# Kernel tuning notes

Hardware: AMD Instinct MI355X
Metric: run time of the kernel (lower is better)

Reference implementation:

```python
import jax, jax.numpy as jnp
import numpy as np

B = 2048   # batch
D = 1280   # backbone feature dim (hardcoded in module)
E = 8      # num_classes == number of expert heads
ALPHA = 0.1
EPS = 1e-5


def _bn(x, g, b, m, v):
    # BatchNorm1d in eval mode: running stats
    return (x - m) * jax.lax.rsqrt(v + EPS) * g + b


def _ln(x, g, b):
    mu = jnp.mean(x, axis=-1, keepdims=True)
    var = jnp.mean((x - mu) ** 2, axis=-1, keepdims=True)
    return (x - mu) * jax.lax.rsqrt(var + EPS) * g + b


@jax.custom_vjp
def _grad_reverse(x):
    return x

def _gr_fwd(x):
    return x, None

def _gr_bwd(_, g):
    return (-ALPHA * g,)

_grad_reverse.defvjp(_gr_fwd, _gr_bwd)


def setup_inputs() -> dict:
    key = jax.random.key(0)
    ks = iter(jax.random.split(key, 80))
    def w(*s):
        return jax.random.normal(next(ks), s, dtype=jnp.float32) * 0.02
    def u(*s):
        return jax.random.uniform(next(ks), s, dtype=jnp.float32) + 0.5
    inp = {"source": jax.random.normal(next(ks), (B, D), dtype=jnp.float32)}
    # bottleneck: Linear(1280,512)+BN+ReLU, Linear(512,256)+BN+ReLU
    inp.update(bw1=w(D, 512), bb1=jnp.zeros(512), bg1=jnp.ones(512), bbe1=jnp.zeros(512), bm1=w(512), bv1=u(512))
    inp.update(bw2=w(512, 256), bb2=jnp.zeros(256), bg2=jnp.ones(256), bbe2=jnp.zeros(256), bm2=w(256), bv2=u(256))
    # source_fc: Linear(256, E) + LogSoftmax
    inp.update(cw=w(256, E), cb=jnp.zeros(E))
    # domain classifier: 1280->1024->1024->512->2 with BN
    inp.update(dw1=w(D, 1024), db1=jnp.zeros(1024), dg1=jnp.ones(1024), dbe1=jnp.zeros(1024), dm1=w(1024), dv1=u(1024))
    inp.update(dw2=w(1024, 1024), db2=jnp.zeros(1024), dg2=jnp.ones(1024), dbe2=jnp.zeros(1024), dm2=w(1024), dv2=u(1024))
    inp.update(dw3=w(1024, 512), db3=jnp.zeros(512), dg3=jnp.ones(512), dbe3=jnp.zeros(512), dm3=w(512), dv3=u(512))
    inp.update(dw4=w(512, 2), db4=jnp.zeros(2))
    # E stacked expert MLPs: 1280->1024->1024->512->2 with LayerNorm
    inp.update(ew1=w(E, D, 1024), eb1=jnp.zeros((E, 1024)), eg1=jnp.ones((E, 1024)), ebe1=jnp.zeros((E, 1024)))
    inp.update(ew2=w(E, 1024, 1024), eb2=jnp.zeros((E, 1024)), eg2=jnp.ones((E, 1024)), ebe2=jnp.zeros((E, 1024)))
    inp.update(ew3=w(E, 1024, 512), eb3=jnp.zeros((E, 512)), eg3=jnp.ones((E, 512)), ebe3=jnp.zeros((E, 512)))
    inp.update(ew4=w(E, 512, 2), eb4=jnp.zeros((E, 2)))
    return inp


def reference(source, bw1, bb1, bg1, bbe1, bm1, bv1, bw2, bb2, bg2, bbe2, bm2, bv2, cw, cb,
              dw1, db1, dg1, dbe1, dm1, dv1, dw2, db2, dg2, dbe2, dm2, dv2,
              dw3, db3, dg3, dbe3, dm3, dv3, dw4, db4,
              ew1, eb1, eg1, ebe1, ew2, eb2, eg2, ebe2, ew3, eb3, eg3, ebe3, ew4, eb4):
    share = source  # sharedNet modeled as identity on extracted features
    # bottleneck + classifier head
    h = jax.nn.relu(_bn(share @ bw1 + bb1, bg1, bbe1, bm1, bv1))
    h = jax.nn.relu(_bn(h @ bw2 + bb2, bg2, bbe2, bm2, bv2))
    src = jax.nn.log_softmax(h @ cw + cb, axis=-1)            # [B, E]
    label = jnp.argmax(src, axis=-1)                          # routing labels (detached by argmax)
    # gradient-reversed features
    rev = _grad_reverse(share)
    # global domain classifier (dropout = identity in eval)
    d = jax.nn.relu(_bn(rev @ dw1 + db1, dg1, dbe1, dm1, dv1))
    d = jax.nn.relu(_bn(d @ dw2 + db2, dg2, dbe2, dm2, dv2))
    d = jax.nn.relu(_bn(d @ dw3 + db3, dg3, dbe3, dm3, dv3))
    dclf = jax.nn.log_softmax(d @ dw4 + db4, axis=-1)         # [B, 2]
    # per-class domain experts: dense all-expert compute + per-sample gather
    x = jax.nn.relu(_ln(jnp.einsum('bd,edh->beh', rev, ew1) + eb1[None], eg1[None], ebe1[None]))
    x = jax.nn.relu(_ln(jnp.einsum('beh,ehk->bek', x, ew2) + eb2[None], eg2[None], ebe2[None]))
    x = jax.nn.relu(_ln(jnp.einsum('beh,ehk->bek', x, ew3) + eb3[None], eg3[None], ebe3[None]))
    eo = jax.nn.log_softmax(jnp.einsum('beh,ehk->bek', x, ew4) + eb4[None], axis=-1)  # [B, E, 2]
    sout = jnp.take_along_axis(eo, label[:, None, None], axis=1)[:, 0, :]             # [B, 2]
    return (src, dclf, sout, share)
```

## Files before the change

### kernel.cpp

```cpp
#include <hip/hip_runtime.h>

typedef unsigned short u16;
typedef short s8v __attribute__((ext_vector_type(8)));
typedef float f4v __attribute__((ext_vector_type(4)));

#define AS1 __attribute__((address_space(1)))
#define AS3 __attribute__((address_space(3)))

__device__ __forceinline__ float bf2f(u16 u) {
    union { unsigned int i; float f; } x; x.i = ((unsigned int)u) << 16; return x.f;
}
__device__ __forceinline__ u16 f2bf(float f) {
    union { float f; unsigned int i; } x; x.f = f;
    unsigned int r = x.i + 0x7fffu + ((x.i >> 16) & 1u);
    return (u16)(r >> 16);
}

__device__ __forceinline__ void glds16(const u16* g, u16* l) {
    __builtin_amdgcn_global_load_lds((AS1 void*)(g), (AS3 void*)(l), 16, 0, 0);
}

__device__ __forceinline__ int swz(int row, int kq) {
    return row * 64 + ((((kq >> 3) ^ row) & 7) << 3);
}

__global__ __launch_bounds__(256) void convT2_k(const float* __restrict__ Wa,
        const float* __restrict__ Wb, int zSplit,
        u16* __restrict__ WT, int N, int K)
{
    const int z = blockIdx.z;
    const float* W = (z < zSplit) ? Wa + (size_t)z * K * N
                                  : Wb + (size_t)(z - zSplit) * K * N;
    WT += (size_t)z * K * N;
    const int n0 = blockIdx.x * 64, k0 = blockIdx.y * 64;
    __shared__ float t[64][65];
    const int r = threadIdx.x >> 2;
    const int c = (threadIdx.x & 3) << 4;
    const float* wp = W + (size_t)(k0 + r) * N + n0 + c;
    #pragma unroll
    for (int q = 0; q < 16; q += 4) {
        float4 f = *(const float4*)(wp + q);
        t[c + q + 0][r] = f.x; t[c + q + 1][r] = f.y;
        t[c + q + 2][r] = f.z; t[c + q + 3][r] = f.w;
    }
    __syncthreads();
    u16* op = WT + (size_t)(n0 + r) * K + k0 + c;
    #pragma unroll
    for (int q = 0; q < 16; q += 8) {
        s8v v;
        #pragma unroll
        for (int j = 0; j < 8; ++j) v[j] = (short)f2bf(t[r][c + q + j]);
        *(s8v*)(op + q) = v;
    }
}

__global__ __launch_bounds__(256) void convsrc_k(const float* __restrict__ in,
        u16* __restrict__ outb, float* __restrict__ outf, int n8)
{
    const int i = blockIdx.x * 256 + threadIdx.x;
    if (i >= n8) return;
    const float4 f0 = ((const float4*)in)[i * 2];
    const float4 f1 = ((const float4*)in)[i * 2 + 1];
    s8v v;
    v[0]=(short)f2bf(f0.x); v[1]=(short)f2bf(f0.y);
    v[2]=(short)f2bf(f0.z); v[3]=(short)f2bf(f0.w);
    v[4]=(short)f2bf(f1.x); v[5]=(short)f2bf(f1.y);
    v[6]=(short)f2bf(f1.z); v[7]=(short)f2bf(f1.w);
    ((s8v*)outb)[i] = v;
    ((float4*)outf)[i * 2]     = f0;
    ((float4*)outf)[i * 2 + 1] = f1;
}

__device__ __forceinline__ void stage_tile(u16* AsH, u16* BsH,
        const u16* ga, const u16* gb, int kk, int ldsq, int K)
{
    #pragma unroll
    for (int q = 0; q < 4; ++q) {
        glds16(ga + kk + (size_t)q * 32 * K, AsH + q * 2048 + ldsq);
        glds16(gb + kk + (size_t)q * 32 * K, BsH + q * 2048 + ldsq);
    }
}

template<int HASDOM>
__global__ __launch_bounds__(256) void gemm_bt128_k(
    const u16* __restrict__ A0, size_t aStrideZ,
    const u16* __restrict__ WT0,
    const float* __restrict__ ebias,
    const float* __restrict__ dbias, const float* __restrict__ dgam,
    const float* __restrict__ dbet,  const float* __restrict__ dmean,
    const float* __restrict__ dvar,  int zdom,
    u16* __restrict__ out0, int M, int N, int K)
{
    const int z = blockIdx.z;
    const u16* A  = A0  + (size_t)z * aStrideZ;
    const u16* WT = WT0 + (size_t)z * N * K;
    u16* out = out0 + (size_t)z * M * N;

    const int n0 = blockIdx.x * 128, m0 = blockIdx.y * 128;
    const int t = threadIdx.x;
    const int w = t >> 6, lane = t & 63;
    const int lq = lane >> 4, lr = lane & 15;
    const int wm = (w >> 1) * 64, wn = (w & 1) * 64;

    __shared__ __align__(16) u16 As[2 * 128 * 64];
    __shared__ __align__(16) u16 Bs[2 * 128 * 64];

    f4v acc[4][4] = {};

    const int schunk = ((t & 7) ^ ((t >> 3) & 7)) << 3;
    const u16* ga = A  + (size_t)(m0 + (t >> 3)) * K + schunk;
    const u16* gb = WT + (size_t)(n0 + (t >> 3)) * K + schunk;
    const int ldsq = w * 512;

    const int NT = K >> 6;
    stage_tile(As, Bs, ga, gb, 0, ldsq, K);
    if (NT > 1) stage_tile(As + 8192, Bs + 8192, ga, gb, 64, ldsq, K);

    for (int tk = 0; tk < NT; ++tk) {
        if (tk < NT - 1) asm volatile("s_waitcnt vmcnt(8)" ::: "memory");
        else             asm volatile("s_waitcnt vmcnt(0)" ::: "memory");
        __builtin_amdgcn_s_barrier();
        __builtin_amdgcn_sched_barrier(0);

        const u16* Ah = As + (tk & 1) * 8192;
        const u16* Bh = Bs + (tk & 1) * 8192;
        __builtin_amdgcn_s_setprio(1);
        #pragma unroll
        for (int ks = 0; ks < 64; ks += 32) {
            const int kq = ks + (lq << 3);
            s8v a[4], b[4];
            #pragma unroll
            for (int i = 0; i < 4; ++i) a[i] = *(const s8v*)&Ah[swz(wm + i*16 + lr, kq)];
            #pragma unroll
            for (int j = 0; j < 4; ++j) b[j] = *(const s8v*)&Bh[swz(wn + j*16 + lr, kq)];
            #pragma unroll
            for (int i = 0; i < 4; ++i)
                #pragma unroll
                for (int j = 0; j < 4; ++j)
                    acc[i][j] = __builtin_amdgcn_mfma_f32_16x16x32_bf16(a[i], b[j], acc[i][j], 0, 0, 0);
        }
        __builtin_amdgcn_s_setprio(0);
        __builtin_amdgcn_sched_barrier(0);
        __builtin_amdgcn_s_barrier();

        if (tk + 2 < NT)
            stage_tile(As + (tk & 1) * 8192, Bs + (tk & 1) * 8192,
                       ga, gb, (tk + 2) << 6, ldsq, K);
    }

    float scale[4], shift[4];
    const bool dom = HASDOM && (z == zdom);
    #pragma unroll
    for (int j = 0; j < 4; ++j) {
        const int c = n0 + wn + j * 16 + lr;
        if (dom) {
            const float s = dgam[c] / sqrtf(dvar[c] + 1e-5f);
            scale[j] = s;
            shift[j] = (dbias[c] - dmean[c]) * s + dbet[c];
        } else {
            scale[j] = 1.f;
            shift[j] = ebias[(size_t)z * N + c];
        }
    }
    const int r0 = lq << 2;
    #pragma unroll
    for (int i = 0; i < 4; ++i) {
        #pragma unroll
        for (int r = 0; r < 4; ++r) {
            const int grow = m0 + wm + i * 16 + r0 + r;
            u16* orow = out + (size_t)grow * N + n0 + wn + lr;
            #pragma unroll
            for (int j = 0; j < 4; ++j) {
                float y = fmaf(acc[i][j][r], scale[j], shift[j]);
                if (dom) y = fmaxf(y, 0.f);
                orow[j * 16] = f2bf(y);
            }
        }
    }
}

__global__ __launch_bounds__(256) void gemm_f32sk_k(
    const float* __restrict__ A, const float* __restrict__ W,
    float* __restrict__ out, int M, int N, int K, int Ks)
{
    const int n0 = blockIdx.x * 64, m0 = blockIdx.y * 64;
    const int kb = blockIdx.z * Ks;
    out += (size_t)blockIdx.z * M * N;
    const int tid = threadIdx.x;
    const int tx = tid & 15, ty = tid >> 4;
    __shared__ float As[64][65];
    __shared__ float Bs[64][64];
    float acc[4][4] = {};
    const int sr = tid >> 2;
    const int sc = (tid & 3) << 4;
    for (int kk = kb; kk < kb + Ks; kk += 64) {
        const float* ap = A + (size_t)(m0 + sr) * K + kk + sc;
        #pragma unroll
        for (int q = 0; q < 4; ++q) {
            float4 f = *(const float4*)(ap + q * 4);
            As[sr][sc + q*4 + 0] = f.x; As[sr][sc + q*4 + 1] = f.y;
            As[sr][sc + q*4 + 2] = f.z; As[sr][sc + q*4 + 3] = f.w;
        }
        const float* wp = W + (size_t)(kk + sr) * N + n0 + sc;
        #pragma unroll
        for (int q = 0; q < 4; ++q)
            *(float4*)&Bs[sr][sc + q*4] = *(const float4*)(wp + q * 4);
        __syncthreads();
        #pragma unroll 4
        for (int kq = 0; kq < 64; ++kq) {
            float a[4], bv[4];
            #pragma unroll
            for (int i = 0; i < 4; ++i) a[i] = As[ty*4 + i][kq];
            #pragma unroll
            for (int j = 0; j < 4; ++j) bv[j] = Bs[kq][tx*4 + j];
            #pragma unroll
            for (int i = 0; i < 4; ++i)
                #pragma unroll
                for (int j = 0; j < 4; ++j)
                    acc[i][j] = fmaf(a[i], bv[j], acc[i][j]);
        }
        __syncthreads();
    }
    #pragma unroll
    for (int j = 0; j < 4; ++j) {
        const int c = n0 + tx*4 + j;
        #pragma unroll
        for (int i = 0; i < 4; ++i)
            out[(size_t)(m0 + ty*4 + i) * N + c] = acc[i][j];
    }
}

__global__ __launch_bounds__(256) void h2gemm_k(
    const float* __restrict__ hp,
    const float* __restrict__ bg1, const float* __restrict__ bbe1,
    const float* __restrict__ bb1, const float* __restrict__ bm1,
    const float* __restrict__ bv1,
    const float* __restrict__ bw2,
    float* __restrict__ out, int B)
{
    const int n0 = blockIdx.x * 64, m0 = blockIdx.y * 64;
    const int kb = blockIdx.z * 128;
    out += (size_t)blockIdx.z * B * 256;
    const size_t sl = (size_t)B * 512;
    const int tid = threadIdx.x;
    const int tx = tid & 15, ty = tid >> 4;
    __shared__ float As[64][65];
    __shared__ float Bs[64][64];
    __shared__ __align__(16) float scl[128], shl[128];
    if (tid < 128) {
        const int k = kb + tid;
        const float sc = bg1[k] / sqrtf(bv1[k] + 1e-5f);
        scl[tid] = sc;
        shl[tid] = (bb1[k] - bm1[k]) * sc + bbe1[k];
    }
    __syncthreads();
    float acc[4][4] = {};
    const int sr = tid >> 2;
    const int sc = (tid & 3) << 4;
    for (int kk = kb; kk < kb + 128; kk += 64) {
        const int kl = kk - kb;
        const float* ap = hp + (size_t)(m0 + sr) * 512 + kk + sc;
        #pragma unroll
        for (int q = 0; q < 4; ++q) {
            const float4 f0 = *(const float4*)(ap + q * 4);
            const float4 f1 = *(const float4*)(ap + sl + q * 4);
            const float4 f2 = *(const float4*)(ap + 2 * sl + q * 4);
            const float4 f3 = *(const float4*)(ap + 3 * sl + q * 4);
            const float4 g = *(const float4*)&scl[kl + sc + q * 4];
            const float4 h = *(const float4*)&shl[kl + sc + q * 4];
            As[sr][sc + q*4 + 0] = fmaxf(fmaf(f0.x + f1.x + f2.x + f3.x, g.x, h.x), 0.f);
            As[sr][sc + q*4 + 1] = fmaxf(fmaf(f0.y + f1.y + f2.y + f3.y, g.y, h.y), 0.f);
            As[sr][sc + q*4 + 2] = fmaxf(fmaf(f0.z + f1.z + f2.z + f3.z, g.z, h.z), 0.f);
            As[sr][sc + q*4 + 3] = fmaxf(fmaf(f0.w + f1.w + f2.w + f3.w, g.w, h.w), 0.f);
        }
        const float* wp = bw2 + (size_t)(kk + sr) * 256 + n0 + sc;
        #pragma unroll
        for (int q = 0; q < 4; ++q)
            *(float4*)&Bs[sr][sc + q*4] = *(const float4*)(wp + q * 4);
        __syncthreads();
        #pragma unroll 4
        for (int kq = 0; kq < 64; ++kq) {
            float a[4], bv[4];
            #pragma unroll
            for (int i = 0; i < 4; ++i) a[i] = As[ty*4 + i][kq];
            #pragma unroll
            for (int j = 0; j < 4; ++j) bv[j] = Bs[kq][tx*4 + j];
            #pragma unroll
            for (int i = 0; i < 4; ++i)
                #pragma unroll
                for (int j = 0; j < 4; ++j)
                    acc[i][j] = fmaf(a[i], bv[j], acc[i][j]);
        }
        __syncthreads();
    }
    #pragma unroll
    for (int j = 0; j < 4; ++j) {
        const int c = n0 + tx*4 + j;
        #pragma unroll
        for (int i = 0; i < 4; ++i)
            out[(size_t)(m0 + ty*4 + i) * 256 + c] = acc[i][j];
    }
}

__global__ __launch_bounds__(256) void cls_k(
    const float* __restrict__ h2p,
    const float* __restrict__ bg2, const float* __restrict__ bbe2,
    const float* __restrict__ bb2, const float* __restrict__ bm2,
    const float* __restrict__ bv2,
    const float* __restrict__ cw,  const float* __restrict__ cb,
    float* __restrict__ out_src, int* __restrict__ label, int B)
{
    const int b = blockIdx.x * 4 + (threadIdx.x >> 6);
    const int lane = threadIdx.x & 63;
    const size_t sl = (size_t)B * 256;
    const float* hb = h2p + (size_t)b * 256 + lane * 4;
    const float4 v0 = *(const float4*)(hb);
    const float4 v1 = *(const float4*)(hb + sl);
    const float4 v2 = *(const float4*)(hb + 2 * sl);
    const float4 v3 = *(const float4*)(hb + 3 * sl);
    const float4 gv = ((const float4*)bg2)[lane];
    const float4 vv = ((const float4*)bv2)[lane];
    const float4 bbv = ((const float4*)bb2)[lane];
    const float4 bmv = ((const float4*)bm2)[lane];
    const float4 bev = ((const float4*)bbe2)[lane];
    float h[4];
    {
        const float s0 = gv.x / sqrtf(vv.x + 1e-5f);
        const float s1 = gv.y / sqrtf(vv.y + 1e-5f);
        const float s2 = gv.z / sqrtf(vv.z + 1e-5f);
        const float s3 = gv.w / sqrtf(vv.w + 1e-5f);
        h[0] = fmaxf(fmaf(v0.x + v1.x + v2.x + v3.x, s0, (bbv.x - bmv.x) * s0 + bev.x), 0.f);
        h[1] = fmaxf(fmaf(v0.y + v1.y + v2.y + v3.y, s1, (bbv.y - bmv.y) * s1 + bev.y), 0.f);
        h[2] = fmaxf(fmaf(v0.z + v1.z + v2.z + v3.z, s2, (bbv.z - bmv.z) * s2 + bev.z), 0.f);
        h[3] = fmaxf(fmaf(v0.w + v1.w + v2.w + v3.w, s3, (bbv.w - bmv.w) * s3 + bev.w), 0.f);
    }
    float p[8] = {};
    #pragma unroll
    for (int j = 0; j < 4; ++j) {
        const float4 c0 = ((const float4*)cw)[(lane * 4 + j) * 2];
        const float4 c1 = ((const float4*)cw)[(lane * 4 + j) * 2 + 1];
        p[0] = fmaf(h[j], c0.x, p[0]); p[1] = fmaf(h[j], c0.y, p[1]);
        p[2] = fmaf(h[j], c0.z, p[2]); p[3] = fmaf(h[j], c0.w, p[3]);
        p[4] = fmaf(h[j], c1.x, p[4]); p[5] = fmaf(h[j], c1.y, p[5]);
        p[6] = fmaf(h[j], c1.z, p[6]); p[7] = fmaf(h[j], c1.w, p[7]);
    }
    #pragma unroll
    for (int off = 32; off; off >>= 1)
        #pragma unroll
        for (int c = 0; c < 8; ++c) p[c] += __shfl_xor(p[c], off, 64);
    if (lane == 0) {
        float lg[8];
        #pragma unroll
        for (int c = 0; c < 8; ++c) lg[c] = p[c] + cb[c];
        float mx = lg[0]; int am = 0;
        #pragma unroll
        for (int c = 1; c < 8; ++c) if (lg[c] > mx) { mx = lg[c]; am = c; }
        float ssum = 0.f;
        #pragma unroll
        for (int c = 0; c < 8; ++c) ssum += expf(lg[c] - mx);
        const float lse = mx + logf(ssum);
        #pragma unroll
        for (int c = 0; c < 8; ++c) out_src[b * 8 + c] = lg[c] - lse;
        label[b] = am;
    }
}

template<int N>
__global__ __launch_bounds__(256) void ln_relu_k(u16* __restrict__ Y,
        const float* __restrict__ g, const float* __restrict__ bb)
{
    const int z = blockIdx.y;
    u16* y = Y + ((size_t)z * gridDim.x + blockIdx.x) * N;
    const float* gz = g  + (size_t)z * N;
    const float* bz = bb + (size_t)z * N;
    const int t = threadIdx.x;
    constexpr int C = N >> 8;
    float vals[C];
    ushort4 u = ((const ushort4*)y)[t];
    vals[0] = bf2f(u.x); vals[1] = bf2f(u.y);
    vals[2] = bf2f(u.z); vals[3] = bf2f(u.w);
    float s = 0.f, sq = 0.f;
    #pragma unroll
    for (int i = 0; i < C; ++i) { s += vals[i]; sq += vals[i] * vals[i]; }
    #pragma unroll
    for (int off = 32; off; off >>= 1) {
        s  += __shfl_xor(s,  off, 64);
        sq += __shfl_xor(sq, off, 64);
    }
    __shared__ float rs[4], rq[4];
    if ((t & 63) == 0) { rs[t >> 6] = s; rq[t >> 6] = sq; }
    __syncthreads();
    s  = rs[0] + rs[1] + rs[2] + rs[3];
    sq = rq[0] + rq[1] + rq[2] + rq[3];
    const float inv = 1.f / (float)N;
    const float mu  = s * inv;
    const float var = sq * inv - mu * mu;
    const float rstd = rsqrtf(var + 1e-5f);
    float4 gv = ((const float4*)gz)[t];
    float4 bv = ((const float4*)bz)[t];
    ushort4 o;
    o.x = f2bf(fmaxf((vals[0] - mu) * rstd * gv.x + bv.x, 0.f));
    o.y = f2bf(fmaxf((vals[1] - mu) * rstd * gv.y + bv.y, 0.f));
    o.z = f2bf(fmaxf((vals[2] - mu) * rstd * gv.z + bv.z, 0.f));
    o.w = f2bf(fmaxf((vals[3] - mu) * rstd * gv.w + bv.w, 0.f));
    ((ushort4*)y)[t] = o;
}

__global__ __launch_bounds__(64) void headsel_k(
    const u16* __restrict__ X,
    const int* __restrict__ label,
    const float* __restrict__ eg3, const float* __restrict__ ebe3,
    const float* __restrict__ ew4, const float* __restrict__ eb4,
    int zBase, float* __restrict__ out_sout, int B)
{
    const int b = blockIdx.x;
    const int e = label[b];
    if (e < zBase || e >= zBase + 4) return;
    const int lane = threadIdx.x;
    const u16* x = X + ((size_t)(e - zBase) * B + b) * 512 + lane * 8;
    uint4 raw = *(const uint4*)x;
    const u16* pu = (const u16*)&raw;
    float v[8];
    #pragma unroll
    for (int i = 0; i < 8; ++i) v[i] = bf2f(pu[i]);
    float s = 0.f, sq = 0.f;
    #pragma unroll
    for (int i = 0; i < 8; ++i) { s += v[i]; sq += v[i] * v[i]; }
    #pragma unroll
    for (int off = 32; off; off >>= 1) {
        s  += __shfl_xor(s,  off, 64);
        sq += __shfl_xor(sq, off, 64);
    }
    const float mu = s * (1.f / 512.f);
    const float var = sq * (1.f / 512.f) - mu * mu;
    const float rstd = rsqrtf(var + 1e-5f);
    const float* g  = eg3  + (size_t)e * 512 + lane * 8;
    const float* be = ebe3 + (size_t)e * 512 + lane * 8;
    const float4 g0 = *(const float4*)g,  g1 = *(const float4*)(g + 4);
    const float4 b0 = *(const float4*)be, b1 = *(const float4*)(be + 4);
    float h[8];
    h[0] = fmaxf((v[0]-mu)*rstd*g0.x + b0.x, 0.f);
    h[1] = fmaxf((v[1]-mu)*rstd*g0.y + b0.y, 0.f);
    h[2] = fmaxf((v[2]-mu)*rstd*g0.z + b0.z, 0.f);
    h[3] = fmaxf((v[3]-mu)*rstd*g0.w + b0.w, 0.f);
    h[4] = fmaxf((v[4]-mu)*rstd*g1.x + b1.x, 0.f);
    h[5] = fmaxf((v[5]-mu)*rstd*g1.y + b1.y, 0.f);
    h[6] = fmaxf((v[6]-mu)*rstd*g1.z + b1.z, 0.f);
    h[7] = fmaxf((v[7]-mu)*rstd*g1.w + b1.w, 0.f);
    const float* W = ew4 + (size_t)e * 1024 + lane * 16;
    float p0 = 0.f, p1 = 0.f;
    #pragma unroll
    for (int q = 0; q < 4; ++q) {
        const float4 wv = *(const float4*)(W + q * 4);
        p0 = fmaf(h[q*2],   wv.x, p0); p1 = fmaf(h[q*2],   wv.y, p1);
        p0 = fmaf(h[q*2+1], wv.z, p0); p1 = fmaf(h[q*2+1], wv.w, p1);
    }
    #pragma unroll
    for (int off = 32; off; off >>= 1) {
        p0 += __shfl_xor(p0, off, 64);
        p1 += __shfl_xor(p1, off, 64);
    }
    if (lane == 0) {
        const float l0 = p0 + eb4[e * 2];
        const float l1 = p1 + eb4[e * 2 + 1];
        const float mx = fmaxf(l0, l1);
        const float lse = mx + logf(expf(l0 - mx) + expf(l1 - mx));
        out_sout[b * 2]     = l0 - lse;
        out_sout[b * 2 + 1] = l1 - lse;
    }
}

__global__ __launch_bounds__(64) void head2_k(const u16* __restrict__ X,
        const float* __restrict__ W, const float* __restrict__ bias,
        float* __restrict__ out)
{
    const int b = blockIdx.x;
    const int lane = threadIdx.x;
    const u16* x = X + (size_t)b * 512 + lane * 8;
    uint4 raw = *(const uint4*)x;
    const u16* pu = (const u16*)&raw;
    const float* Wz = W + lane * 16;
    float p0 = 0.f, p1 = 0.f;
    #pragma unroll
    for (int q = 0; q < 4; ++q) {
        const float4 wv = *(const float4*)(Wz + q * 4);
        p0 = fmaf(bf2f(pu[q*2]),   wv.x, p0); p1 = fmaf(bf2f(pu[q*2]),   wv.y, p1);
        p0 = fmaf(bf2f(pu[q*2+1]), wv.z, p0); p1 = fmaf(bf2f(pu[q*2+1]), wv.w, p1);
    }
    #pragma unroll
    for (int off = 32; off; off >>= 1) {
        p0 += __shfl_xor(p0, off, 64);
        p1 += __shfl_xor(p1, off, 64);
    }
    if (lane == 0) {
        const float l0 = p0 + bias[0];
        const float l1 = p1 + bias[1];
        const float mx = fmaxf(l0, l1);
        const float lse = mx + logf(expf(l0 - mx) + expf(l1 - mx));
        out[b * 2]     = l0 - lse;
        out[b * 2 + 1] = l1 - lse;
    }
}


extern "C" void kernel_launch(void* const* d_in, const int* in_sizes, int n_in,
                              void* d_out, int out_size, void* d_ws, size_t ws_size,
                              hipStream_t stream)
{
    const int B = 2048, D = 1280, E = 8;

    const float* src = (const float*)d_in[0];
    const float *bw1 = (const float*)d_in[1],  *bb1 = (const float*)d_in[2],
                *bg1 = (const float*)d_in[3],  *bbe1 = (const float*)d_in[4],
                *bm1 = (const float*)d_in[5],  *bv1 = (const float*)d_in[6];
    const float *bw2 = (const float*)d_in[7],  *bb2 = (const float*)d_in[8],
                *bg2 = (const float*)d_in[9],  *bbe2 = (const float*)d_in[10],
                *bm2 = (const float*)d_in[11], *bv2 = (const float*)d_in[12];
    const float *cw  = (const float*)d_in[13], *cb  = (const float*)d_in[14];
    const float *dw1 = (const float*)d_in[15], *db1 = (const float*)d_in[16],
                *dg1 = (const float*)d_in[17], *dbe1 = (const float*)d_in[18],
                *dm1 = (const float*)d_in[19], *dv1 = (const float*)d_in[20];
    const float *dw2 = (const float*)d_in[21], *db2 = (const float*)d_in[22],
                *dg2 = (const float*)d_in[23], *dbe2 = (const float*)d_in[24],
                *dm2 = (const float*)d_in[25], *dv2 = (const float*)d_in[26];
    const float *dw3 = (const float*)d_in[27], *db3 = (const float*)d_in[28],
                *dg3 = (const float*)d_in[29], *dbe3 = (const float*)d_in[30],
                *dm3 = (const float*)d_in[31], *dv3 = (const float*)d_in[32];
    const float *dw4 = (const float*)d_in[33], *db4 = (const float*)d_in[34];
    const float *ew1 = (const float*)d_in[35], *eb1 = (const float*)d_in[36],
                *eg1 = (const float*)d_in[37], *ebe1 = (const float*)d_in[38];
    const float *ew2 = (const float*)d_in[39], *eb2 = (const float*)d_in[40],
                *eg2 = (const float*)d_in[41], *ebe2 = (const float*)d_in[42];
    const float *ew3 = (const float*)d_in[43], *eb3 = (const float*)d_in[44],
                *eg3 = (const float*)d_in[45], *ebe3 = (const float*)d_in[46];
    const float *ew4 = (const float*)d_in[47], *eb4 = (const float*)d_in[48];

    float* out_src   = (float*)d_out;
    float* out_dclf  = out_src + B * E;
    float* out_sout  = out_dclf + B * 2;
    float* out_share = out_sout + B * 2;

    char* ws = (char*)d_ws;
    u16*   wslot = (u16*)ws;
    u16*   srcb  = (u16*)(ws + 13107200);
    u16*   acta  = (u16*)(ws + 18350080);
    u16*   actb  = (u16*)(ws + 39321600);
    int*   label = (int*)(ws + 60293120);
    float* hp    = (float*)(ws + 18350080);
    float* h2p   = (float*)(ws);

    const size_t s1024 = (size_t)B * 1024, s512 = (size_t)B * 512;

    convsrc_k<<<dim3(B * D / 8 / 256), 256, 0, stream>>>(src, srcb, out_share, B * D / 8);

    gemm_f32sk_k<<<dim3(512 / 64, B / 64, 4), 256, 0, stream>>>(
        src, bw1, hp, B, 512, D, 320);
    h2gemm_k<<<dim3(256 / 64, B / 64, 4), 256, 0, stream>>>(
        hp, bg1, bbe1, bb1, bm1, bv1, bw2, h2p, B);
    cls_k<<<dim3(B / 4), 256, 0, stream>>>(
        h2p, bg2, bbe2, bb2, bm2, bv2, cw, cb, out_src, label, B);

    convT2_k<<<dim3(16, 20, 5), 256, 0, stream>>>(ew1, dw1, 4, wslot, 1024, 1280);
    gemm_bt128_k<1><<<dim3(8, 16, 5), 256, 0, stream>>>(
        srcb, 0, wslot, eb1, db1, dg1, dbe1, dm1, dv1, 4, acta, B, 1024, 1280);
    ln_relu_k<1024><<<dim3(B, 4), 256, 0, stream>>>(acta, eg1, ebe1);

    convT2_k<<<dim3(16, 16, 5), 256, 0, stream>>>(ew2, dw2, 4, wslot, 1024, 1024);
    gemm_bt128_k<1><<<dim3(8, 16, 5), 256, 0, stream>>>(
        acta, s1024, wslot, eb2, db2, dg2, dbe2, dm2, dv2, 4, actb, B, 1024, 1024);
    ln_relu_k<1024><<<dim3(B, 4), 256, 0, stream>>>(actb, eg2, ebe2);

    convT2_k<<<dim3(8, 16, 5), 256, 0, stream>>>(ew3, dw3, 4, wslot, 512, 1024);
    gemm_bt128_k<1><<<dim3(4, 16, 5), 256, 0, stream>>>(
        actb, s1024, wslot, eb3, db3, dg3, dbe3, dm3, dv3, 4, acta, B, 512, 1024);

    headsel_k<<<dim3(B), 64, 0, stream>>>(
        acta, label, eg3, ebe3, ew4, eb4, 0, out_sout, B);
    head2_k<<<dim3(B), 64, 0, stream>>>(
        acta + (size_t)4 * s512, dw4, db4, out_dclf);

    convT2_k<<<dim3(16, 20, 4), 256, 0, stream>>>(
        ew1 + (size_t)4*1280*1024, ew1 + (size_t)4*1280*1024, 4, wslot, 1024, 1280);
    gemm_bt128_k<0><<<dim3(8, 16, 4), 256, 0, stream>>>(
        srcb, 0, wslot, eb1 + (size_t)4*1024,
        nullptr, nullptr, nullptr, nullptr, nullptr, -1, acta, B, 1024, 1280);
    ln_relu_k<1024><<<dim3(B, 4), 256, 0, stream>>>(acta, eg1 + (size_t)4*1024, ebe1 + (size_t)4*1024);

    convT2_k<<<dim3(16, 16, 4), 256, 0, stream>>>(
        ew2 + (size_t)4*1024*1024, ew2 + (size_t)4*1024*1024, 4, wslot, 1024, 1024);
    gemm_bt128_k<0><<<dim3(8, 16, 4), 256, 0, stream>>>(
        acta, s1024, wslot, eb2 + (size_t)4*1024,
        nullptr, nullptr, nullptr, nullptr, nullptr, -1, actb, B, 1024, 1024);
    ln_relu_k<1024><<<dim3(B, 4), 256, 0, stream>>>(actb, eg2 + (size_t)4*1024, ebe2 + (size_t)4*1024);

    convT2_k<<<dim3(8, 16, 4), 256, 0, stream>>>(
        ew3 + (size_t)4*1024*512, ew3 + (size_t)4*1024*512, 4, wslot, 512, 1024);
    gemm_bt128_k<0><<<dim3(4, 16, 4), 256, 0, stream>>>(
        actb, s1024, wslot, eb3 + (size_t)4*512,
        nullptr, nullptr, nullptr, nullptr, nullptr, -1, acta, B, 512, 1024);

    headsel_k<<<dim3(B), 64, 0, stream>>>(
        acta, label, eg3, ebe3, ew4, eb4, 4, out_sout, B);
}
```

Baseline: 552.4 us.

## Use 8-wave blocks for bf16 GEMM and widen fp32 split-K tile

```diff
diff --git a/kernel.cpp b/kernel.cpp
--- a/kernel.cpp
+++ b/kernel.cpp
@@ -71,18 +71,8 @@
     ((float4*)outf)[i * 2 + 1] = f1;
 }
 
-__device__ __forceinline__ void stage_tile(u16* AsH, u16* BsH,
-        const u16* ga, const u16* gb, int kk, int ldsq, int K)
-{
-    #pragma unroll
-    for (int q = 0; q < 4; ++q) {
-        glds16(ga + kk + (size_t)q * 32 * K, AsH + q * 2048 + ldsq);
-        glds16(gb + kk + (size_t)q * 32 * K, BsH + q * 2048 + ldsq);
-    }
-}
-
 template<int HASDOM>
-__global__ __launch_bounds__(256) void gemm_bt128_k(
+__global__ __launch_bounds__(512) void gemm_bt128_k(
     const u16* __restrict__ A0, size_t aStrideZ,
     const u16* __restrict__ WT0,
     const float* __restrict__ ebias,
@@ -100,24 +90,33 @@
     const int t = threadIdx.x;
     const int w = t >> 6, lane = t & 63;
     const int lq = lane >> 4, lr = lane & 15;
-    const int wm = (w >> 1) * 64, wn = (w & 1) * 64;
+    const int wm = (w >> 1) * 32;
+    const int wn = (w & 1) * 64;
 
     __shared__ __align__(16) u16 As[2 * 128 * 64];
     __shared__ __align__(16) u16 Bs[2 * 128 * 64];
 
-    f4v acc[4][4] = {};
-
-    const int schunk = ((t & 7) ^ ((t >> 3) & 7)) << 3;
-    const u16* ga = A  + (size_t)(m0 + (t >> 3)) * K + schunk;
-    const u16* gb = WT + (size_t)(n0 + (t >> 3)) * K + schunk;
-    const int ldsq = w * 512;
+    f4v acc[2][4] = {};
+
+    const int srow = t >> 3;
+    const u16* ga = A  + (size_t)(m0 + srow) * K + (((t & 7) ^ (srow & 7)) << 3);
+    const u16* gb = WT + (size_t)(n0 + srow) * K + (((t & 7) ^ (srow & 7)) << 3);
+    const int wq = w * 512;
+    const int rowK = 64 * K;
+
+#define STAGE(buf, kk) do { \
+    glds16(ga + (kk),        As + (buf) * 8192 + wq); \
+    glds16(ga + (kk) + rowK, As + (buf) * 8192 + 4096 + wq); \
+    glds16(gb + (kk),        Bs + (buf) * 8192 + wq); \
+    glds16(gb + (kk) + rowK, Bs + (buf) * 8192 + 4096 + wq); \
+  } while (0)
 
     const int NT = K >> 6;
-    stage_tile(As, Bs, ga, gb, 0, ldsq, K);
-    if (NT > 1) stage_tile(As + 8192, Bs + 8192, ga, gb, 64, ldsq, K);
+    STAGE(0, 0);
+    STAGE(1, 64);
 
     for (int tk = 0; tk < NT; ++tk) {
-        if (tk < NT - 1) asm volatile("s_waitcnt vmcnt(8)" ::: "memory");
+        if (tk < NT - 1) asm volatile("s_waitcnt vmcnt(4)" ::: "memory");
         else             asm volatile("s_waitcnt vmcnt(0)" ::: "memory");
         __builtin_amdgcn_s_barrier();
         __builtin_amdgcn_sched_barrier(0);
@@ -128,13 +127,13 @@
         #pragma unroll
         for (int ks = 0; ks < 64; ks += 32) {
             const int kq = ks + (lq << 3);
-            s8v a[4], b[4];
-            #pragma unroll
-            for (int i = 0; i < 4; ++i) a[i] = *(const s8v*)&Ah[swz(wm + i*16 + lr, kq)];
+            s8v a[2], b[4];
+            #pragma unroll
+            for (int i = 0; i < 2; ++i) a[i] = *(const s8v*)&Ah[swz(wm + i*16 + lr, kq)];
             #pragma unroll
             for (int j = 0; j < 4; ++j) b[j] = *(const s8v*)&Bh[swz(wn + j*16 + lr, kq)];
             #pragma unroll
-            for (int i = 0; i < 4; ++i)
+            for (int i = 0; i < 2; ++i)
                 #pragma unroll
                 for (int j = 0; j < 4; ++j)
                     acc[i][j] = __builtin_amdgcn_mfma_f32_16x16x32_bf16(a[i], b[j], acc[i][j], 0, 0, 0);
@@ -144,9 +143,9 @@
         __builtin_amdgcn_s_barrier();
 
         if (tk + 2 < NT)
-            stage_tile(As + (tk & 1) * 8192, Bs + (tk & 1) * 8192,
-                       ga, gb, (tk + 2) << 6, ldsq, K);
-    }
+            STAGE(tk & 1, (tk + 2) << 6);
+    }
+#undef STAGE
 
     float scale[4], shift[4];
     const bool dom = HASDOM && (z == zdom);
@@ -164,7 +163,7 @@
     }
     const int r0 = lq << 2;
     #pragma unroll
-    for (int i = 0; i < 4; ++i) {
+    for (int i = 0; i < 2; ++i) {
         #pragma unroll
         for (int r = 0; r < 4; ++r) {
             const int grow = m0 + wm + i * 16 + r0 + r;
@@ -183,50 +182,56 @@
     const float* __restrict__ A, const float* __restrict__ W,
     float* __restrict__ out, int M, int N, int K, int Ks)
 {
-    const int n0 = blockIdx.x * 64, m0 = blockIdx.y * 64;
+    const int n0 = blockIdx.x * 128, m0 = blockIdx.y * 64;
     const int kb = blockIdx.z * Ks;
     out += (size_t)blockIdx.z * M * N;
-    const int tid = threadIdx.x;
-    const int tx = tid & 15, ty = tid >> 4;
-    __shared__ float As[64][65];
-    __shared__ float Bs[64][64];
-    float acc[4][4] = {};
-    const int sr = tid >> 2;
-    const int sc = (tid & 3) << 4;
-    for (int kk = kb; kk < kb + Ks; kk += 64) {
-        const float* ap = A + (size_t)(m0 + sr) * K + kk + sc;
-        #pragma unroll
-        for (int q = 0; q < 4; ++q) {
-            float4 f = *(const float4*)(ap + q * 4);
-            As[sr][sc + q*4 + 0] = f.x; As[sr][sc + q*4 + 1] = f.y;
-            As[sr][sc + q*4 + 2] = f.z; As[sr][sc + q*4 + 3] = f.w;
-        }
-        const float* wp = W + (size_t)(kk + sr) * N + n0 + sc;
+    const int t = threadIdx.x;
+    const int tx = t & 15, ty = t >> 4;
+    __shared__ float As[64 * 33];
+    __shared__ float Bs[32 * 132];
+    float acc[4][8] = {};
+    const int ar = t >> 2, akc = (t & 3) * 8;
+    const int bk = t >> 3, bnc = (t & 7) * 16;
+    for (int kk = kb; kk < kb + Ks; kk += 32) {
+        const float* ap = A + (size_t)(m0 + ar) * K + kk + akc;
+        const float4 fa0 = *(const float4*)(ap);
+        const float4 fa1 = *(const float4*)(ap + 4);
+        float* asp = &As[ar * 33 + akc];
+        asp[0] = fa0.x; asp[1] = fa0.y; asp[2] = fa0.z; asp[3] = fa0.w;
+        asp[4] = fa1.x; asp[5] = fa1.y; asp[6] = fa1.z; asp[7] = fa1.w;
+        const float* wp = W + (size_t)(kk + bk) * N + n0 + bnc;
         #pragma unroll
         for (int q = 0; q < 4; ++q)
-            *(float4*)&Bs[sr][sc + q*4] = *(const float4*)(wp + q * 4);
+            *(float4*)&Bs[bk * 132 + bnc + q * 4] = *(const float4*)(wp + q * 4);
         __syncthreads();
-        #pragma unroll 4
-        for (int kq = 0; kq < 64; ++kq) {
-            float a[4], bv[4];
-            #pragma unroll
-            for (int i = 0; i < 4; ++i) a[i] = As[ty*4 + i][kq];
-            #pragma unroll
-            for (int j = 0; j < 4; ++j) bv[j] = Bs[kq][tx*4 + j];
-            #pragma unroll
-            for (int i = 0; i < 4; ++i)
-                #pragma unroll
-                for (int j = 0; j < 4; ++j)
-                    acc[i][j] = fmaf(a[i], bv[j], acc[i][j]);
+        #pragma unroll 8
+        for (int kq = 0; kq < 32; ++kq) {
+            float a[4];
+            #pragma unroll
+            for (int i = 0; i < 4; ++i) a[i] = As[(ty + 16 * i) * 33 + kq];
+            const float4 b0 = *(const float4*)&Bs[kq * 132 + tx * 4];
+            const float4 b1 = *(const float4*)&Bs[kq * 132 + tx * 4 + 64];
+            #pragma unroll
+            for (int i = 0; i < 4; ++i) {
+                acc[i][0] = fmaf(a[i], b0.x, acc[i][0]);
+                acc[i][1] = fmaf(a[i], b0.y, acc[i][1]);
+                acc[i][2] = fmaf(a[i], b0.z, acc[i][2]);
+                acc[i][3] = fmaf(a[i], b0.w, acc[i][3]);
+                acc[i][4] = fmaf(a[i], b1.x, acc[i][4]);
+                acc[i][5] = fmaf(a[i], b1.y, acc[i][5]);
+                acc[i][6] = fmaf(a[i], b1.z, acc[i][6]);
+                acc[i][7] = fmaf(a[i], b1.w, acc[i][7]);
+            }
         }
         __syncthreads();
     }
     #pragma unroll
-    for (int j = 0; j < 4; ++j) {
-        const int c = n0 + tx*4 + j;
-        #pragma unroll
-        for (int i = 0; i < 4; ++i)
-            out[(size_t)(m0 + ty*4 + i) * N + c] = acc[i][j];
+    for (int i = 0; i < 4; ++i) {
+        float* orow = out + (size_t)(m0 + ty + 16 * i) * N + n0 + tx * 4;
+        float4 o0; o0.x = acc[i][0]; o0.y = acc[i][1]; o0.z = acc[i][2]; o0.w = acc[i][3];
+        float4 o1; o1.x = acc[i][4]; o1.y = acc[i][5]; o1.z = acc[i][6]; o1.w = acc[i][7];
+        *(float4*)orow = o0;
+        *(float4*)(orow + 64) = o1;
     }
 }
 
@@ -553,7 +558,7 @@
 
     convsrc_k<<<dim3(B * D / 8 / 256), 256, 0, stream>>>(src, srcb, out_share, B * D / 8);
 
-    gemm_f32sk_k<<<dim3(512 / 64, B / 64, 4), 256, 0, stream>>>(
+    gemm_f32sk_k<<<dim3(512 / 128, B / 64, 4), 256, 0, stream>>>(
         src, bw1, hp, B, 512, D, 320);
     h2gemm_k<<<dim3(256 / 64, B / 64, 4), 256, 0, stream>>>(
         hp, bg1, bbe1, bb1, bm1, bv1, bw2, h2p, B);
@@ -561,17 +566,17 @@
         h2p, bg2, bbe2, bb2, bm2, bv2, cw, cb, out_src, label, B);
 
     convT2_k<<<dim3(16, 20, 5), 256, 0, stream>>>(ew1, dw1, 4, wslot, 1024, 1280);
-    gemm_bt128_k<1><<<dim3(8, 16, 5), 256, 0, stream>>>(
+    gemm_bt128_k<1><<<dim3(8, 16, 5), 512, 0, stream>>>(
         srcb, 0, wslot, eb1, db1, dg1, dbe1, dm1, dv1, 4, acta, B, 1024, 1280);
     ln_relu_k<1024><<<dim3(B, 4), 256, 0, stream>>>(acta, eg1, ebe1);
 
     convT2_k<<<dim3(16, 16, 5), 256, 0, stream>>>(ew2, dw2, 4, wslot, 1024, 1024);
-    gemm_bt128_k<1><<<dim3(8, 16, 5), 256, 0, stream>>>(
+    gemm_bt128_k<1><<<dim3(8, 16, 5), 512, 0, stream>>>(
         acta, s1024, wslot, eb2, db2, dg2, dbe2, dm2, dv2, 4, actb, B, 1024, 1024);
     ln_relu_k<1024><<<dim3(B, 4), 256, 0, stream>>>(actb, eg2, ebe2);
 
     convT2_k<<<dim3(8, 16, 5), 256, 0, stream>>>(ew3, dw3, 4, wslot, 512, 1024);
-    gemm_bt128_k<1><<<dim3(4, 16, 5), 256, 0, stream>>>(
+    gemm_bt128_k<1><<<dim3(4, 16, 5), 512, 0, stream>>>(
         actb, s1024, wslot, eb3, db3, dg3, dbe3, dm3, dv3, 4, acta, B, 512, 1024);
 
     headsel_k<<<dim3(B), 64, 0, stream>>>(
@@ -581,21 +586,21 @@
 
     convT2_k<<<dim3(16, 20, 4), 256, 0, stream>>>(
         ew1 + (size_t)4*1280*1024, ew1 + (size_t)4*1280*1024, 4, wslot, 1024, 1280);
-    gemm_bt128_k<0><<<dim3(8, 16, 4), 256, 0, stream>>>(
+    gemm_bt128_k<0><<<dim3(8, 16, 4), 512, 0, stream>>>(
         srcb, 0, wslot, eb1 + (size_t)4*1024,
         nullptr, nullptr, nullptr, nullptr, nullptr, -1, acta, B, 1024, 1280);
     ln_relu_k<1024><<<dim3(B, 4), 256, 0, stream>>>(acta, eg1 + (size_t)4*1024, ebe1 + (size_t)4*1024);
 
     convT2_k<<<dim3(16, 16, 4), 256, 0, stream>>>(
         ew2 + (size_t)4*1024*1024, ew2 + (size_t)4*1024*1024, 4, wslot, 1024, 1024);
-    gemm_bt128_k<0><<<dim3(8, 16, 4), 256, 0, stream>>>(
+    gemm_bt128_k<0><<<dim3(8, 16, 4), 512, 0, stream>>>(
         acta, s1024, wslot, eb2 + (size_t)4*1024,
         nullptr, nullptr, nullptr, nullptr, nullptr, -1, actb, B, 1024, 1024);
     ln_relu_k<1024><<<dim3(B, 4), 256, 0, stream>>>(actb, eg2 + (size_t)4*1024, ebe2 + (size_t)4*1024);
 
     convT2_k<<<dim3(8, 16, 4), 256, 0, stream>>>(
         ew3 + (size_t)4*1024*512, ew3 + (size_t)4*1024*512, 4, wslot, 512, 1024);
-    gemm_bt128_k<0><<<dim3(4, 16, 4), 256, 0, stream>>>(
+    gemm_bt128_k<0><<<dim3(4, 16, 4), 512, 0, stream>>>(
         actb, s1024, wslot, eb3 + (size_t)4*512,
         nullptr, nullptr, nullptr, nullptr, nullptr, -1, acta, B, 512, 1024);
 
```

Measured after the change: 540.6 us, median of 2. 2.1% less time.
